# Optimization experiments

Measured on AMD Instinct MI355X. Metric: run time of the kernel, lower is better.

The kernel has to match this reference:

```python
import jax, jax.numpy as jnp
import numpy as np

POS_THRESH = 0.5
NEG_THRESH = 0.3
MIN_ANCHOR = 3
N_ANCHOR = 500000
N_GT = 200


def _iou_matrix(a, g):
    # a: [N,4], g: [M,4], boxes as (x1,y1,x2,y2)
    area_a = (a[:, 2] - a[:, 0]) * (a[:, 3] - a[:, 1])          # [N]
    area_g = (g[:, 2] - g[:, 0]) * (g[:, 3] - g[:, 1])          # [M]
    lt = jnp.maximum(a[:, None, :2], g[None, :, :2])            # [N,M,2]
    rb = jnp.minimum(a[:, None, 2:], g[None, :, 2:])            # [N,M,2]
    wh = jnp.clip(rb - lt, 0.0)
    inter = wh[..., 0] * wh[..., 1]                              # [N,M]
    return inter / (area_a[:, None] + area_g[None, :] - inter)


def _make_boxes(key, n, coord_max, size_min, size_max):
    kc, ks = jax.random.split(key)
    c = jax.random.uniform(kc, (n, 2), jnp.float32, 0.0, coord_max)
    s = jax.random.uniform(ks, (n, 2), jnp.float32, size_min, size_max)
    return jnp.concatenate([c - 0.5 * s, c + 0.5 * s], axis=1)


def setup_inputs() -> dict:
    key = jax.random.key(0)
    ka, kg = jax.random.split(key)
    anchor = _make_boxes(ka, N_ANCHOR, 1024.0, 8.0, 128.0)
    gt = _make_boxes(kg, N_GT, 1024.0, 16.0, 256.0)
    return {"anchor": anchor, "gt": gt}


def reference(anchor, gt):
    n, m = anchor.shape[0], gt.shape[0]
    iou_mat = _iou_matrix(anchor, gt)                            # [N,M]
    max_iou = jnp.max(iou_mat, axis=1)                           # [N]
    max_idx = jnp.argmax(iou_mat, axis=1).astype(jnp.int32)      # [N] (first max, like torch)
    assign = jnp.full((n,), -2, dtype=jnp.int32)
    assign = jnp.where(max_iou < NEG_THRESH, -1, assign)
    assign = jnp.where(max_iou > POS_THRESH, max_idx, assign)

    # per-GT top-k anchors (iou_mat.T : [M,N])
    vals, ranks = jax.lax.top_k(iou_mat.T, MIN_ANCHOR)           # [M,K]
    low = jnp.sum(vals > POS_THRESH, axis=1) < MIN_ANCHOR        # [M] gt lacking enough positives
    # claim[m,k]: gt m claims anchor ranks[m,k]. k==0 always (best anchor forced);
    # others only if gt is low-quality and iou > 0.1
    claim = (jnp.arange(MIN_ANCHOR)[None, :] == 0) | (low[:, None] & (vals > 0.1))
    gt_idx = jnp.broadcast_to(jnp.arange(m, dtype=jnp.int32)[:, None], (m, MIN_ANCHOR))
    claim_val = jnp.where(claim, gt_idx, -1)                     # [M,K]
    # original python loop runs gt idx in increasing order, later overwrites earlier
    # -> final winner for a contested anchor is the MAX claiming gt index: scatter-max
    forced = jnp.full((n,), -1, dtype=jnp.int32).at[ranks.reshape(-1)].max(claim_val.reshape(-1))
    assign = jnp.where(forced >= 0, forced, assign)
    return assign
```

## Files before the change

### kernel.cpp

```cpp
#include <hip/hip_runtime.h>
#include <stdint.h>


typedef unsigned int u32;
typedef unsigned char u8;
typedef unsigned long long u64;

#define POS_THRESH 0.5f
#define NEG_THRESH 0.3f
#define CLAIM_THRESH 0.1f

constexpr int NCX = 32, NCY = 32, NCELL = NCX * NCY;
constexpr float INV_CELL = 0.03125f;
constexpr float MARGIN = 64.5f;
constexpr int MPAD = 256;
constexpr int HSLOTS = 1024;
constexpr int GRID_MAIN = 1024;
constexpr int TPB_MAIN = 512;
constexpr int NSHADOW = 16;
constexpr int SSTRIDE = 8;

#define IOU_EVAL(a, areaA, g, areaG, inter, iou) {                \
    float ltx = fmaxf(a.x, g.x), lty = fmaxf(a.y, g.y);           \
    float rbx = fminf(a.z, g.z), rby = fminf(a.w, g.w);           \
    float ww = fmaxf(rbx - ltx, 0.0f);                            \
    float hh = fmaxf(rby - lty, 0.0f);                            \
    inter = ww * hh;                                              \
    iou = 0.0f;                                                   \
    if (inter > 0.0f) iou = inter / ((areaA + areaG) - inter);    \
}

#define INS3(t0, t1, t2, k) do {                                  \
    if ((k) > (t2)) {                                             \
        if ((k) > (t0))      { t2 = t1; t1 = t0; t0 = (k); }      \
        else if ((k) > (t1)) { t2 = t1; t1 = (k); }               \
        else                 { t2 = (k); }                        \
    } } while (0)

__device__ __forceinline__ int cell_of(const float4 a) {
    float cx = 0.5f * (a.x + a.z);
    float cy = 0.5f * (a.y + a.w);
    int ix = (int)(cx * INV_CELL);
    int iy = (int)(cy * INV_CELL);
    ix = ix < 0 ? 0 : (ix > NCX - 1 ? NCX - 1 : ix);
    iy = iy < 0 ? 0 : (iy > NCY - 1 ? NCY - 1 : iy);
    return iy * NCX + ix;
}

__device__ __forceinline__ void gt_range(const float4 g, int& clx, int& chx,
                                         int& cly, int& chy) {
    clx = (int)floorf((g.x - MARGIN) * INV_CELL);
    chx = (int)floorf((g.z + MARGIN) * INV_CELL);
    cly = (int)floorf((g.y - MARGIN) * INV_CELL);
    chy = (int)floorf((g.w + MARGIN) * INV_CELL);
    clx = clx < 0 ? 0 : (clx > NCX - 1 ? NCX - 1 : clx);
    chx = chx < 0 ? 0 : (chx > NCX - 1 ? NCX - 1 : chx);
    cly = cly < 0 ? 0 : (cly > NCY - 1 ? NCY - 1 : cly);
    chy = chy < 0 ? 0 : (chy > NCY - 1 ? NCY - 1 : chy);
}

#define CASCADE3(p0, p1, p2, key) {                               \
    u64 x_ = (key);                                               \
    u64 o_ = atomicMax(&(p0), x_); x_ = o_ < x_ ? o_ : x_;        \
    o_ = atomicMax(&(p1), x_); x_ = o_ < x_ ? o_ : x_;            \
    atomicMax(&(p2), x_);                                         \
}

__global__ void __launch_bounds__(256) k_prep(
    const float4* __restrict__ gt, u32* __restrict__ gtCnt,
    u8* __restrict__ gtIds, u64* __restrict__ shadow3, int M)
{
    __shared__ u32 l_cnt[NCELL];
    const int tid = threadIdx.x;
    for (int c = tid; c < NCELL; c += 256) l_cnt[c] = 0;
    __syncthreads();

    for (int e = tid; e < M * NSHADOW; e += 256) {
        u64* slot = shadow3 + (size_t)e * SSTRIDE;
        slot[0] = 0; slot[1] = 0; slot[2] = 0;
    }

    if (tid < M) {
        float4 g = gt[tid];
        int clx, chx, cly, chy;
        gt_range(g, clx, chx, cly, chy);
        for (int iy = cly; iy <= chy; ++iy)
            for (int ix = clx; ix <= chx; ++ix) {
                int c = iy * NCX + ix;
                u32 slot = atomicAdd(&l_cnt[c], 1u);
                gtIds[(size_t)c * M + slot] = (u8)tid;
            }
    }
    __syncthreads();
    for (int c = tid; c < NCELL; c += 256) gtCnt[c] = l_cnt[c];
}

__global__ void __launch_bounds__(TPB_MAIN) k_main(
    const float4* __restrict__ anchor, const float4* __restrict__ gt,
    const u32* __restrict__ gtCnt, const u8* __restrict__ gtIds,
    u64* __restrict__ shadow3, int* __restrict__ out, int N, int M)
{
    __shared__ float4 s_g[MPAD];
    __shared__ float  s_ga[MPAD];
    __shared__ u64    tbl[3 * MPAD];
    const int tid = threadIdx.x;

    if (tid < M) {
        float4 g = gt[tid];
        s_g[tid]  = g;
        s_ga[tid] = (g.z - g.x) * (g.w - g.y);
    }
    for (int e = tid; e < 3 * MPAD; e += TPB_MAIN) tbl[e] = 0;
    __syncthreads();

    for (int i = blockIdx.x * TPB_MAIN + tid; i < N;
         i += TPB_MAIN * GRID_MAIN) {
        float4 a = anchor[i];
        float area_a = (a.z - a.x) * (a.w - a.y);
        int c   = cell_of(a);
        int cnt = (int)gtCnt[c];
        const u8* list = gtIds + (size_t)c * M;
        u32 nai = ~(u32)i;

        u64 best = 0;
        for (int k = 0; k < cnt; ++k) {
            int m = list[k];
            float4 g = s_g[m];
            float inter, iou;
            IOU_EVAL(a, area_a, g, s_ga[m], inter, iou);
            if (inter > 0.0f) {
                u32 ib = __float_as_uint(iou);
                u64 kb = ((u64)ib << 32) | (~(u32)m);
                best = kb > best ? kb : best;
                u64 kt = ((u64)ib << 32) | nai;
                if (kt > tbl[m * 3 + 2])
                    CASCADE3(tbl[m * 3 + 0], tbl[m * 3 + 1], tbl[m * 3 + 2], kt);
            }
        }
        u32 ib = (u32)(best >> 32);
        int v = -2;
        if (ib < __float_as_uint(NEG_THRESH)) v = -1;
        if (ib > __float_as_uint(POS_THRESH)) v = (int)(~(u32)best);
        out[i] = v;
    }
    __syncthreads();

    const int s = blockIdx.x & (NSHADOW - 1);
    for (int e = tid; e < 3 * M; e += TPB_MAIN) {
        u64 v = tbl[e];
        if ((u32)(v >> 32) == 0) continue;
        int m = e / 3;
        u64* g3 = shadow3 + ((size_t)m * NSHADOW + s) * SSTRIDE;
        if (v <= g3[2]) continue;
        CASCADE3(g3[0], g3[1], g3[2], v);
    }
}

__global__ void __launch_bounds__(256) k_claims(
    const u64* __restrict__ shadow3, int* __restrict__ out, int M)
{
    __shared__ u64 s_key[3 * MPAD];
    __shared__ u64 h_val[HSLOTS];
    __shared__ u32 h_tag[HSLOTS];
    const int tid = threadIdx.x;

    for (int i = tid; i < HSLOTS; i += 256) { h_val[i] = 0; h_tag[i] = 0; }

    if (tid < M) {
        u64 q0 = 0x00000000FFFFFFFFULL;
        u64 q1 = 0x00000000FFFFFFFEULL;
        u64 q2 = 0x00000000FFFFFFFDULL;
        const u64* base = shadow3 + (size_t)tid * NSHADOW * SSTRIDE;
        for (int s = 0; s < NSHADOW; ++s) {
            const u64* p = base + (size_t)s * SSTRIDE;
            INS3(q0, q1, q2, p[0]);
            INS3(q0, q1, q2, p[1]);
            INS3(q0, q1, q2, p[2]);
        }

        float v0 = __uint_as_float((u32)(q0 >> 32));
        float v1 = __uint_as_float((u32)(q1 >> 32));
        float v2 = __uint_as_float((u32)(q2 >> 32));
        u32 a0 = ~(u32)q0;
        u32 a1 = ~(u32)q1;
        u32 a2 = ~(u32)q2;

        int npos = (v0 > POS_THRESH) + (v1 > POS_THRESH) + (v2 > POS_THRESH);
        bool low = npos < 3;

        s_key[tid * 3 + 0] = ((u64)a0 << 32) | (u32)(tid + 1);
        s_key[tid * 3 + 1] = (low && v1 > CLAIM_THRESH)
            ? (((u64)a1 << 32) | (u32)(tid + 1)) : 0ULL;
        s_key[tid * 3 + 2] = (low && v2 > CLAIM_THRESH)
            ? (((u64)a2 << 32) | (u32)(tid + 1)) : 0ULL;
    }
    __syncthreads();

    const int tote = 3 * M;
    for (int e = tid; e < tote; e += 256) {
        u64 my = s_key[e];
        if (my == 0) continue;
        u32 myA = (u32)(my >> 32);
        u32 slot = (myA * 2654435761u) & (HSLOTS - 1);
        while (true) {
            u32 prev = atomicCAS(&h_tag[slot], 0u, myA + 1u);
            if (prev == 0u || prev == myA + 1u) {
                atomicMax(&h_val[slot], my);
                break;
            }
            slot = (slot + 1) & (HSLOTS - 1);
        }
    }
    __syncthreads();
    for (int e = tid; e < tote; e += 256) {
        u64 my = s_key[e];
        if (my == 0) continue;
        u32 myA = (u32)(my >> 32);
        u32 slot = (myA * 2654435761u) & (HSLOTS - 1);
        while (h_tag[slot] != myA + 1u) slot = (slot + 1) & (HSLOTS - 1);
        if (h_val[slot] == my) out[myA] = (int)(my & 0xffffffffULL) - 1;
    }
}

extern "C" void kernel_launch(void* const* d_in, const int* in_sizes, int n_in,
                              void* d_out, int out_size, void* d_ws, size_t ws_size,
                              hipStream_t stream) {
    const float4* anchor = (const float4*)d_in[0];
    const float4* gt     = (const float4*)d_in[1];
    int N = in_sizes[0] / 4;
    int M = in_sizes[1] / 4;
    int* out = (int*)d_out;

    char* ws = (char*)d_ws;
    size_t off = 0;
    auto alloc = [&](size_t bytes, size_t align) -> void* {
        off = (off + align - 1) / align * align;
        void* p = ws + off;
        off += bytes;
        return p;
    };
    u32* gtCnt   = (u32*)alloc(NCELL * 4, 64);
    u64* shadow3 = (u64*)alloc((size_t)MPAD * NSHADOW * SSTRIDE * 8, 64);
    u8*  gtIds   = (u8*)alloc((size_t)NCELL * M, 1);

    k_prep<<<1, 256, 0, stream>>>(gt, gtCnt, gtIds, shadow3, M);
    k_main<<<GRID_MAIN, TPB_MAIN, 0, stream>>>(anchor, gt, gtCnt, gtIds,
                                               shadow3, out, N, M);
    k_claims<<<1, 256, 0, stream>>>(shadow3, out, M);
}
```

Baseline: 123.7 us.

## Bin anchors by grid cell and process one cell per block

Adds a scatter pass that bins anchor indices by spatial cell using atomic cursors. The main kernel then runs one block per cell, loading only that cell's GT boxes into shared memory and indexing them compactly. The goal is to remove divergent per-anchor cell lists and avoid the full-M shared table, so the top-3 table holds only that cell's GTs. The cost is an extra kernel, scattered anchor gathers and output writes, and a fixed per-cell capacity (CAP=2048) that could overflow if anchors are denser than expected.

```diff
diff --git a/kernel.cpp b/kernel.cpp
--- a/kernel.cpp
+++ b/kernel.cpp
@@ -15,10 +15,10 @@
 constexpr float MARGIN = 64.5f;
 constexpr int MPAD = 256;
 constexpr int HSLOTS = 1024;
-constexpr int GRID_MAIN = 1024;
-constexpr int TPB_MAIN = 512;
 constexpr int NSHADOW = 16;
 constexpr int SSTRIDE = 8;
+constexpr int CPAD = 16;
+constexpr int CAP = 2048;
 
 #define IOU_EVAL(a, areaA, g, areaG, inter, iou) {                \
     float ltx = fmaxf(a.x, g.x), lty = fmaxf(a.y, g.y);           \
@@ -68,17 +68,19 @@
 
 __global__ void __launch_bounds__(256) k_prep(
     const float4* __restrict__ gt, u32* __restrict__ gtCnt,
-    u8* __restrict__ gtIds, u64* __restrict__ shadow3, int M)
+    u8* __restrict__ gtIds, u32* __restrict__ cursor,
+    u64* __restrict__ shadow3, int M)
 {
     __shared__ u32 l_cnt[NCELL];
     const int tid = threadIdx.x;
     for (int c = tid; c < NCELL; c += 256) l_cnt[c] = 0;
-    __syncthreads();
-
+
+    for (int e = tid; e < NCELL * CPAD; e += 256) cursor[e] = 0;
     for (int e = tid; e < M * NSHADOW; e += 256) {
         u64* slot = shadow3 + (size_t)e * SSTRIDE;
         slot[0] = 0; slot[1] = 0; slot[2] = 0;
     }
+    __syncthreads();
 
     if (tid < M) {
         float4 g = gt[tid];
@@ -88,68 +90,84 @@
             for (int ix = clx; ix <= chx; ++ix) {
                 int c = iy * NCX + ix;
                 u32 slot = atomicAdd(&l_cnt[c], 1u);
-                gtIds[(size_t)c * M + slot] = (u8)tid;
+                gtIds[(size_t)c * MPAD + slot] = (u8)tid;
             }
     }
     __syncthreads();
     for (int c = tid; c < NCELL; c += 256) gtCnt[c] = l_cnt[c];
 }
 
-__global__ void __launch_bounds__(TPB_MAIN) k_main(
+__global__ void __launch_bounds__(256) k_scatidx(
+    const float4* __restrict__ anchor, u32* __restrict__ cursor,
+    int* __restrict__ binnedIdx, int N)
+{
+    int i = blockIdx.x * 256 + threadIdx.x;
+    if (i >= N) return;
+    int c = cell_of(anchor[i]);
+    u32 pos = atomicAdd(&cursor[c * CPAD], 1u);
+    binnedIdx[(size_t)c * CAP + pos] = i;
+}
+
+__global__ void __launch_bounds__(256) k_walk(
     const float4* __restrict__ anchor, const float4* __restrict__ gt,
     const u32* __restrict__ gtCnt, const u8* __restrict__ gtIds,
-    u64* __restrict__ shadow3, int* __restrict__ out, int N, int M)
-{
-    __shared__ float4 s_g[MPAD];
+    const u32* __restrict__ cursor, const int* __restrict__ binnedIdx,
+    u64* __restrict__ shadow3, int* __restrict__ out, int M)
+{
+    __shared__ float4 s_gb[MPAD];
     __shared__ float  s_ga[MPAD];
+    __shared__ int    s_id[MPAD];
     __shared__ u64    tbl[3 * MPAD];
+    const int c   = blockIdx.x;
     const int tid = threadIdx.x;
-
-    if (tid < M) {
-        float4 g = gt[tid];
-        s_g[tid]  = g;
+    const int cnt = (int)gtCnt[c];
+
+    if (tid < cnt) {
+        int m = gtIds[(size_t)c * MPAD + tid];
+        float4 g = gt[m];
+        s_gb[tid] = g;
         s_ga[tid] = (g.z - g.x) * (g.w - g.y);
-    }
-    for (int e = tid; e < 3 * MPAD; e += TPB_MAIN) tbl[e] = 0;
-    __syncthreads();
-
-    for (int i = blockIdx.x * TPB_MAIN + tid; i < N;
-         i += TPB_MAIN * GRID_MAIN) {
-        float4 a = anchor[i];
+        s_id[tid] = m;
+    }
+    for (int e = tid; e < 3 * MPAD; e += 256) tbl[e] = 0;
+    const int nA = (int)cursor[c * CPAD];
+    __syncthreads();
+
+    for (int p = tid; p < nA; p += 256) {
+        int idx = binnedIdx[(size_t)c * CAP + p];
+        float4 a = anchor[idx];
         float area_a = (a.z - a.x) * (a.w - a.y);
-        int c   = cell_of(a);
-        int cnt = (int)gtCnt[c];
-        const u8* list = gtIds + (size_t)c * M;
-        u32 nai = ~(u32)i;
+        u32 nai = ~(u32)idx;
 
         u64 best = 0;
         for (int k = 0; k < cnt; ++k) {
-            int m = list[k];
-            float4 g = s_g[m];
+            float4 g = s_gb[k];
+            float ag = s_ga[k];
             float inter, iou;
-            IOU_EVAL(a, area_a, g, s_ga[m], inter, iou);
+            IOU_EVAL(a, area_a, g, ag, inter, iou);
             if (inter > 0.0f) {
                 u32 ib = __float_as_uint(iou);
-                u64 kb = ((u64)ib << 32) | (~(u32)m);
+                u64 kb = ((u64)ib << 32) | (~(u32)s_id[k]);
                 best = kb > best ? kb : best;
                 u64 kt = ((u64)ib << 32) | nai;
-                if (kt > tbl[m * 3 + 2])
-                    CASCADE3(tbl[m * 3 + 0], tbl[m * 3 + 1], tbl[m * 3 + 2], kt);
+                if (kt > tbl[k * 3 + 2])
+                    CASCADE3(tbl[k * 3 + 0], tbl[k * 3 + 1],
+                             tbl[k * 3 + 2], kt);
             }
         }
         u32 ib = (u32)(best >> 32);
         int v = -2;
         if (ib < __float_as_uint(NEG_THRESH)) v = -1;
         if (ib > __float_as_uint(POS_THRESH)) v = (int)(~(u32)best);
-        out[i] = v;
+        out[idx] = v;
     }
     __syncthreads();
 
     const int s = blockIdx.x & (NSHADOW - 1);
-    for (int e = tid; e < 3 * M; e += TPB_MAIN) {
+    for (int e = tid; e < 3 * cnt; e += 256) {
         u64 v = tbl[e];
         if ((u32)(v >> 32) == 0) continue;
-        int m = e / 3;
+        int m = s_id[e / 3];
         u64* g3 = shadow3 + ((size_t)m * NSHADOW + s) * SSTRIDE;
         if (v <= g3[2]) continue;
         CASCADE3(g3[0], g3[1], g3[2], v);
@@ -239,12 +257,16 @@
         off += bytes;
         return p;
     };
-    u32* gtCnt   = (u32*)alloc(NCELL * 4, 64);
-    u64* shadow3 = (u64*)alloc((size_t)MPAD * NSHADOW * SSTRIDE * 8, 64);
-    u8*  gtIds   = (u8*)alloc((size_t)NCELL * M, 1);
-
-    k_prep<<<1, 256, 0, stream>>>(gt, gtCnt, gtIds, shadow3, M);
-    k_main<<<GRID_MAIN, TPB_MAIN, 0, stream>>>(anchor, gt, gtCnt, gtIds,
-                                               shadow3, out, N, M);
+    u32* gtCnt     = (u32*)alloc(NCELL * 4, 64);
+    u32* cursor    = (u32*)alloc((size_t)NCELL * CPAD * 4, 64);
+    u64* shadow3   = (u64*)alloc((size_t)MPAD * NSHADOW * SSTRIDE * 8, 64);
+    u8*  gtIds     = (u8*)alloc((size_t)NCELL * MPAD, 16);
+    int* binnedIdx = (int*)alloc((size_t)NCELL * CAP * 4, 16);
+
+    int nb = (N + 255) / 256;
+    k_prep<<<1, 256, 0, stream>>>(gt, gtCnt, gtIds, cursor, shadow3, M);
+    k_scatidx<<<nb, 256, 0, stream>>>(anchor, cursor, binnedIdx, N);
+    k_walk<<<NCELL, 256, 0, stream>>>(anchor, gt, gtCnt, gtIds, cursor,
+                                      binnedIdx, shadow3, out, M);
     k_claims<<<1, 256, 0, stream>>>(shadow3, out, M);
 }
```

After: 261.7 us. +111.6%, slower.
